# Kernel tuning notes

Measured on AMD Instinct MI355X. Metric: run time of the kernel, lower is better.

## Reference

```python
import jax, jax.numpy as jnp
import numpy as np

B, T, D, H = 4, 2048, 1024, 16
HD = D // H  # head_size = 64


def setup_inputs() -> dict:
    key = jax.random.key(0)
    ks = jax.random.split(key, 6)
    s = 0.02
    x = jax.random.normal(ks[0], (B, T, D), dtype=jnp.float32)
    # per-head unfused projections, stacked over heads: [H, D, HD]
    Wq = jax.random.normal(ks[1], (H, D, HD), dtype=jnp.float32) * s
    Wk = jax.random.normal(ks[2], (H, D, HD), dtype=jnp.float32) * s
    Wv = jax.random.normal(ks[3], (H, D, HD), dtype=jnp.float32) * s
    # output projection, torch Linear layout [out, in]
    Wo = jax.random.normal(ks[4], (D, D), dtype=jnp.float32) * s
    bo = jax.random.normal(ks[5], (D,), dtype=jnp.float32) * s
    return {"x": x, "Wq": Wq, "Wk": Wk, "Wv": Wv, "Wo": Wo, "bo": bo}


def reference(x, Wq, Wk, Wv, Wo, bo):
    b, t, d = x.shape
    hd = Wq.shape[-1]
    q = jnp.einsum('btd,hdk->bhtk', x, Wq)
    k = jnp.einsum('btd,hdk->bhtk', x, Wk)
    v = jnp.einsum('btd,hdk->bhtk', x, Wv)
    scores = jnp.einsum('bhtk,bhsk->bhts', q, k) / jnp.sqrt(jnp.float32(hd))
    mask = jnp.tril(jnp.ones((t, t), dtype=bool))  # causal
    scores = jnp.where(mask, scores, jnp.float32(-jnp.inf))
    p = jax.nn.softmax(scores, axis=-1)
    o = jnp.einsum('bhts,bhsk->bhtk', p, v)
    o = o.transpose(0, 2, 1, 3).reshape(b, t, d)  # concat heads
    return o @ Wo.T + bo
```

## Files before the change

kernel.cpp:

```cpp
#include <hip/hip_runtime.h>
#include <hip/hip_bf16.h>
#include <stdint.h>

#define B_   4
#define T_   2048
#define D_   1024
#define H_   16
#define HD_  64
#define MROWS (B_*T_)
#define NQKV  3072
#define NST  (T_/64)

typedef __attribute__((ext_vector_type(8))) short  short8;
typedef __attribute__((ext_vector_type(4))) short  bf16x4;
typedef __attribute__((ext_vector_type(4))) float  floatx4;

#define QSCALE 0.1803368801111244f

__device__ inline void async_copy16(const __hip_bfloat16* g, __hip_bfloat16* l) {
  __builtin_amdgcn_global_load_lds(
      (const __attribute__((address_space(1))) void*)g,
      (__attribute__((address_space(3))) void*)l, 16, 0, 0);
}

__device__ inline floatx4 mfma16(bf16x4 a, bf16x4 b, floatx4 c) {
#if __has_builtin(__builtin_amdgcn_mfma_f32_16x16x16bf16_1k)
  return __builtin_amdgcn_mfma_f32_16x16x16bf16_1k(a, b, c, 0, 0, 0);
#elif __has_builtin(__builtin_amdgcn_mfma_f32_16x16x16_bf16)
  return __builtin_amdgcn_mfma_f32_16x16x16_bf16(a, b, c, 0, 0, 0);
#else
  short8 a8 = (short8){a[0], a[1], a[2], a[3], 0, 0, 0, 0};
  short8 b8 = (short8){b[0], b[1], b[2], b[3], 0, 0, 0, 0};
  return __builtin_amdgcn_mfma_f32_16x16x32_bf16(a8, b8, c, 0, 0, 0);
#endif
}

__global__ void prep(const float* __restrict__ x, const float* __restrict__ Wo,
                     const float* __restrict__ Wq, const float* __restrict__ Wk,
                     const float* __restrict__ Wv,
                     __hip_bfloat16* __restrict__ xb, __hip_bfloat16* __restrict__ wob,
                     __hip_bfloat16* __restrict__ wqkv) {
  __shared__ __hip_bfloat16 tile[64][65];
  const int bid = (int)blockIdx.x;
  const int t = threadIdx.x;
  if (bid < 8192) {
    int i = (bid * 256 + t) * 4;
    float4 v = *(const float4*)(x + i);
    xb[i + 0] = __float2bfloat16(v.x);
    xb[i + 1] = __float2bfloat16(v.y);
    xb[i + 2] = __float2bfloat16(v.z);
    xb[i + 3] = __float2bfloat16(v.w);
  } else if (bid < 9216) {
    int i = ((bid - 8192) * 256 + t) * 4;
    float4 v = *(const float4*)(Wo + i);
    wob[i + 0] = __float2bfloat16(v.x);
    wob[i + 1] = __float2bfloat16(v.y);
    wob[i + 2] = __float2bfloat16(v.z);
    wob[i + 3] = __float2bfloat16(v.w);
  } else {
    int idx = bid - 9216;
    const int d0 = (idx & 15) * 64;
    const int wh = idx >> 4;
    const int which = wh >> 4, h = wh & 15;
    const float* W = (which == 0) ? Wq : ((which == 1) ? Wk : Wv);
    const float* base = W + (size_t)h * D_ * HD_;
#pragma unroll
    for (int i = 0; i < 16; i++) {
      int e = i * 256 + t;
      int dr = e >> 6, hd = e & 63;
      tile[dr][hd] = __float2bfloat16(base[(size_t)(d0 + dr) * HD_ + hd]);
    }
    __syncthreads();
#pragma unroll
    for (int i = 0; i < 16; i++) {
      int e = i * 256 + t;
      int hd = e >> 6, dr = e & 63;
      wqkv[(size_t)(which * 1024 + h * 64 + hd) * D_ + d0 + dr] = tile[dr][hd];
    }
  }
}

__global__ void repack_kv(const __hip_bfloat16* __restrict__ qkv,
                          __hip_bfloat16* __restrict__ kpack, __hip_bfloat16* __restrict__ vpack) {
  __shared__ __hip_bfloat16 Ks[64][72];
  __shared__ __hip_bfloat16 Vs[64][72];
  const int tid = threadIdx.x;
  const int st = blockIdx.x, bh = blockIdx.y;
  const int b = bh >> 4, h = bh & 15;
#pragma unroll
  for (int p = 0; p < 2; p++) {
    int c = p * 256 + tid;
    int row = c >> 3, col8 = c & 7;
    const __hip_bfloat16* src = qkv + (size_t)(b * T_ + st * 64 + row) * NQKV + h * HD_ + col8 * 8;
    *(uint4*)&Ks[row][col8 * 8] = *(const uint4*)(src + 1024);
    *(uint4*)&Vs[row][col8 * 8] = *(const uint4*)(src + 2048);
  }
  __syncthreads();
  const size_t base = ((size_t)bh * NST + st) * 8 * 512;
#pragma unroll
  for (int p = 0; p < 2; p++) {
    int pair = p * 256 + tid;
    int c = pair >> 6, l = pair & 63;
    int lq = l & 15, q = l >> 4;
    int ni = c >> 1, half = c & 1;
    short8 v = *(const short8*)&Ks[ni * 16 + lq][half * 32 + q * 8];
    *(short8*)(kpack + base + (size_t)c * 512 + l * 8) = v;
  }
#pragma unroll
  for (int p = 0; p < 2; p++) {
    int pair = p * 256 + tid;
    int c = pair >> 6, l = pair & 63;
    int lq = l & 15, q = l >> 4;
    int m = c >> 2, nt = c & 3;
    __hip_bfloat16 tmp[8];
#pragma unroll
    for (int half = 0; half < 2; half++)
#pragma unroll
      for (int j = 0; j < 4; j++)
        tmp[half * 4 + j] = Vs[(2 * m + half) * 16 + q * 4 + j][nt * 16 + lq];
    *(short8*)(vpack + base + (size_t)c * 512 + l * 8) = *(short8*)tmp;
  }
}


__device__ inline void stage16k(const __hip_bfloat16* __restrict__ grow0, int K,
                                short* ldst, int tid) {
#pragma unroll
  for (int l = 0; l < 2; ++l) {
    int c = l * 512 + tid;
    int r = c >> 3;
    int sw = (c & 7) ^ (r & 7);
    async_copy16(grow0 + (size_t)r * K + sw * 8, (__hip_bfloat16*)(ldst + c * 8));
  }
}

__device__ inline short8 fragld2(const short* base, int r, int slot) {
  return *(const short8*)(base + r * 64 + (((slot) ^ (r & 7)) << 3));
}

__launch_bounds__(512, 2)
__global__ void gemmq(const __hip_bfloat16* __restrict__ A, const __hip_bfloat16* __restrict__ Bt,
                      __hip_bfloat16* __restrict__ Cb, int M, int N, int K, float qscale) {
  __shared__ short LDS[2][32768];
  const int tid = threadIdx.x;
  const int lane = tid & 63, wid = tid >> 6;
  const int lq = lane & 15, quad = lane >> 4;
  const int wr = wid >> 2, wc = wid & 3;

  const int lin = (int)blockIdx.x;
  const int s = (lin & 7) * 64 + (lin >> 3);
  const int m0 = (s & 63) * 128, n0 = (s >> 6) * 384;

  const int NT = K >> 6;

  floatx4 acc[4][6];
#pragma unroll
  for (int i = 0; i < 4; i++)
#pragma unroll
    for (int j = 0; j < 6; j++) acc[i][j] = (floatx4){0.f, 0.f, 0.f, 0.f};

  {
    short* b0 = &LDS[0][0];
    stage16k(A + (size_t)m0 * K, K, b0, tid);
#pragma unroll
    for (int j = 0; j < 3; ++j)
      stage16k(Bt + (size_t)(n0 + 128 * j) * K, K, b0 + 8192 + 8192 * j, tid);
  }

#pragma unroll 1
  for (int t = 0; t < NT; ++t) {
    __syncthreads();
    const short* buf = &LDS[t & 1][0];
    short* nb = &LDS[(t & 1) ^ 1][0];
    const int kc = (t + 1) << 6;

    short8 a0[4], b0[6];
#pragma unroll
    for (int mi = 0; mi < 4; ++mi)
      a0[mi] = fragld2(buf, wr * 64 + mi * 16 + lq, quad);
#pragma unroll
    for (int ni = 0; ni < 6; ++ni)
      b0[ni] = fragld2(buf + 8192, wc * 96 + ni * 16 + lq, quad);
    if (t + 1 < NT) {
      stage16k(A + (size_t)m0 * K + kc, K, nb, tid);
#pragma unroll
      for (int j = 0; j < 3; ++j)
        stage16k(Bt + (size_t)(n0 + 128 * j) * K + kc, K, nb + 8192 + 8192 * j, tid);
    }
    __builtin_amdgcn_s_setprio(1);
#pragma unroll
    for (int mi = 0; mi < 4; ++mi)
#pragma unroll
      for (int ni = 0; ni < 6; ++ni)
        acc[mi][ni] = __builtin_amdgcn_mfma_f32_16x16x32_bf16(a0[mi], b0[ni], acc[mi][ni], 0, 0, 0);
    __builtin_amdgcn_s_setprio(0);

    short8 a1[4], b1[6];
#pragma unroll
    for (int mi = 0; mi < 4; ++mi)
      a1[mi] = fragld2(buf, wr * 64 + mi * 16 + lq, 4 + quad);
#pragma unroll
    for (int ni = 0; ni < 6; ++ni)
      b1[ni] = fragld2(buf + 8192, wc * 96 + ni * 16 + lq, 4 + quad);
    __builtin_amdgcn_s_setprio(1);
#pragma unroll
    for (int mi = 0; mi < 4; ++mi)
#pragma unroll
      for (int ni = 0; ni < 6; ++ni)
        acc[mi][ni] = __builtin_amdgcn_mfma_f32_16x16x32_bf16(a1[mi], b1[ni], acc[mi][ni], 0, 0, 0);
    __builtin_amdgcn_s_setprio(0);
  }

#pragma unroll
  for (int mi = 0; mi < 4; ++mi) {
#pragma unroll
    for (int ni = 0; ni < 6; ++ni) {
      int col = n0 + wc * 96 + ni * 16 + lq;
      float sc = (col < 1024) ? qscale : 1.0f;
#pragma unroll
      for (int r = 0; r < 4; ++r) {
        int row = m0 + wr * 64 + mi * 16 + quad * 4 + r;
        Cb[(size_t)row * N + col] = __float2bfloat16(acc[mi][ni][r] * sc);
      }
    }
  }
}

template <int EPI>
__launch_bounds__(256, 2)
__global__ void gemm_bt(const __hip_bfloat16* __restrict__ A, const __hip_bfloat16* __restrict__ Bt,
                        __hip_bfloat16* __restrict__ Cb, float* __restrict__ Cf,
                        const float* __restrict__ bias, int M, int N, int K, float qscale) {
  __shared__ __hip_bfloat16 As[128 * 32];
  __shared__ __hip_bfloat16 Bs[128 * 32];
  const int tid = threadIdx.x;
  const int w = tid >> 6, lane = tid & 63;
  const int lq = lane & 15, quad = lane >> 4;
  const int wr = w >> 1, wc = w & 1;
  const int m0 = blockIdx.x * 128, n0 = blockIdx.y * 128;

  floatx4 acc[4][4];
#pragma unroll
  for (int i = 0; i < 4; i++)
#pragma unroll
    for (int j = 0; j < 4; j++) acc[i][j] = (floatx4){0.f, 0.f, 0.f, 0.f};

  for (int k0 = 0; k0 < K; k0 += 32) {
    __syncthreads();
#pragma unroll
    for (int ph = 0; ph < 2; ++ph) {
      int c = ph * 256 + tid;
      int row = c >> 2, col8 = c & 3;
      async_copy16(A + (size_t)(m0 + row) * K + k0 + col8 * 8, As + c * 8);
      async_copy16(Bt + (size_t)(n0 + row) * K + k0 + col8 * 8, Bs + c * 8);
    }
    __syncthreads();
    short8 af[4], bf[4];
#pragma unroll
    for (int mi = 0; mi < 4; mi++)
      af[mi] = *(const short8*)(As + (wr * 64 + mi * 16 + lq) * 32 + quad * 8);
#pragma unroll
    for (int ni = 0; ni < 4; ni++)
      bf[ni] = *(const short8*)(Bs + (wc * 64 + ni * 16 + lq) * 32 + quad * 8);
#pragma unroll
    for (int mi = 0; mi < 4; mi++)
#pragma unroll
      for (int ni = 0; ni < 4; ni++)
        acc[mi][ni] = __builtin_amdgcn_mfma_f32_16x16x32_bf16(af[mi], bf[ni], acc[mi][ni], 0, 0, 0);
  }

#pragma unroll
  for (int mi = 0; mi < 4; mi++) {
#pragma unroll
    for (int ni = 0; ni < 4; ni++) {
      int col = n0 + wc * 64 + ni * 16 + lq;
      if (EPI == 0) {
        float s = (col < 1024) ? qscale : 1.0f;
#pragma unroll
        for (int r = 0; r < 4; r++) {
          int row = m0 + wr * 64 + mi * 16 + quad * 4 + r;
          Cb[(size_t)row * N + col] = __float2bfloat16(acc[mi][ni][r] * s);
        }
      } else {
        float bv = bias[col];
#pragma unroll
        for (int r = 0; r < 4; r++) {
          int row = m0 + wr * 64 + mi * 16 + quad * 4 + r;
          Cf[(size_t)row * N + col] = acc[mi][ni][r] + bv;
        }
      }
    }
  }
}

__launch_bounds__(256, 2)
__global__ void attn(const __hip_bfloat16* __restrict__ qkv,
                     const __hip_bfloat16* __restrict__ kpack,
                     const __hip_bfloat16* __restrict__ vpack,
                     __hip_bfloat16* __restrict__ obuf) {
  __shared__ __hip_bfloat16 KVs[2][8192];
  const int tid = threadIdx.x;
  const int w = tid >> 6, lane = tid & 63;
  const int lq = lane & 15, quad = lane >> 4;

  const int bh = (int)blockIdx.x;
  const int a  = (int)blockIdx.y;
  const int b = bh >> 4, h = bh & 15;

  const __hip_bfloat16* kbase = kpack + ((size_t)bh * NST) * 4096;
  const __hip_bfloat16* vbase = vpack + ((size_t)bh * NST) * 4096;

#pragma unroll 1
  for (int seg = 0; seg < 2; ++seg) {
    const int tbase = seg ? (NST - 2 - 2 * a) : (2 * a);
    const int qt = tbase + (w >> 1);
    const int rbase = (w & 1) * 32;

    short8 qf[2][2];
#pragma unroll
    for (int bi = 0; bi < 2; bi++) {
      const __hip_bfloat16* qp =
          qkv + ((size_t)(b * T_ + qt * 64 + rbase + bi * 16 + lq)) * NQKV + h * HD_;
      qf[bi][0] = *(const short8*)(qp + quad * 8);
      qf[bi][1] = *(const short8*)(qp + 32 + quad * 8);
    }

    floatx4 Oacc[2][4];
#pragma unroll
    for (int bi = 0; bi < 2; bi++)
#pragma unroll
      for (int i = 0; i < 4; i++) Oacc[bi][i] = (floatx4){0.f, 0.f, 0.f, 0.f};
    float lrow[2] = {0.f, 0.f};

    const int itTop = tbase + 1;

#pragma unroll
    for (int j = 0; j < 2; ++j) {
      int c = j * 256 + tid;
      async_copy16(kbase + (size_t)c * 8, &KVs[0][0] + c * 8);
      async_copy16(vbase + (size_t)c * 8, &KVs[0][4096] + c * 8);
    }
    __syncthreads();

#pragma unroll 1
    for (int it = 0; it <= itTop; ++it) {
      const int cur = it & 1;
      if (it < itTop) {
        const __hip_bfloat16* kn = kbase + (size_t)(it + 1) * 4096;
        const __hip_bfloat16* vn = vbase + (size_t)(it + 1) * 4096;
#pragma unroll
        for (int j = 0; j < 2; ++j) {
          int c = j * 256 + tid;
          async_copy16(kn + (size_t)c * 8, &KVs[cur ^ 1][0] + c * 8);
          async_copy16(vn + (size_t)c * 8, &KVs[cur ^ 1][4096] + c * 8);
        }
      }
      if (it <= qt) {
        const __hip_bfloat16* Kb = &KVs[cur][0] + lane * 8;
        const __hip_bfloat16* Vb = &KVs[cur][4096] + lane * 8;
        short8 kf[4], kg[4];
#pragma unroll
        for (int ni = 0; ni < 4; ni++) {
          kf[ni] = *(const short8*)(Kb + (size_t)(ni * 2 + 0) * 512);
          kg[ni] = *(const short8*)(Kb + (size_t)(ni * 2 + 1) * 512);
        }
        short8 vfr[8];
#pragma unroll
        for (int c = 0; c < 8; c++) vfr[c] = *(const short8*)(Vb + (size_t)c * 512);

        floatx4 Sc[2][4];
        __builtin_amdgcn_s_setprio(1);
#pragma unroll
        for (int bi = 0; bi < 2; bi++)
#pragma unroll
          for (int ni = 0; ni < 4; ni++) {
            floatx4 c0 = (floatx4){0.f, 0.f, 0.f, 0.f};
            c0 = __builtin_amdgcn_mfma_f32_16x16x32_bf16(kf[ni], qf[bi][0], c0, 0, 0, 0);
            c0 = __builtin_amdgcn_mfma_f32_16x16x32_bf16(kg[ni], qf[bi][1], c0, 0, 0, 0);
            Sc[bi][ni] = c0;
          }
        __builtin_amdgcn_s_setprio(0);

        if (it == qt) {
#pragma unroll
          for (int bi = 0; bi < 2; bi++) {
            int lrow_idx = rbase + bi * 16 + lq;
#pragma unroll
            for (int ni = 0; ni < 4; ni++)
#pragma unroll
              for (int r = 0; r < 4; r++) {
                int s_loc = ni * 16 + quad * 4 + r;
                if (s_loc > lrow_idx) Sc[bi][ni][r] = -__builtin_inff();
              }
          }
        }

        bf16x4 pf[2][4];
#pragma unroll
        for (int bi = 0; bi < 2; bi++)
#pragma unroll
          for (int c = 0; c < 4; c++) {
            __hip_bfloat16 pb[4];
#pragma unroll
            for (int r = 0; r < 4; r++) {
              float p = __builtin_amdgcn_exp2f(Sc[bi][c][r]);
              lrow[bi] += p;
              pb[r] = __float2bfloat16(p);
            }
            pf[bi][c] = *(bf16x4*)pb;
          }

        __builtin_amdgcn_s_setprio(1);
#pragma unroll
        for (int m = 0; m < 2; m++)
#pragma unroll
          for (int nt = 0; nt < 4; nt++) {
            short8 v8 = vfr[m * 4 + nt];
            bf16x4 vlo = (bf16x4){v8[0], v8[1], v8[2], v8[3]};
            bf16x4 vhi = (bf16x4){v8[4], v8[5], v8[6], v8[7]};
#pragma unroll
            for (int bi = 0; bi < 2; bi++) {
              Oacc[bi][nt] = mfma16(pf[bi][2 * m + 0], vlo, Oacc[bi][nt]);
              Oacc[bi][nt] = mfma16(pf[bi][2 * m + 1], vhi, Oacc[bi][nt]);
            }
          }
        __builtin_amdgcn_s_setprio(0);
      }
      __syncthreads();
    }

#pragma unroll
    for (int bi = 0; bi < 2; bi++) {
      float ps = lrow[bi];
      ps += __shfl_xor(ps, 16);
      ps += __shfl_xor(ps, 32);
      float inv = 1.0f / ps;
#pragma unroll
      for (int r = 0; r < 4; r++) {
        float invr = __shfl(inv, quad * 4 + r);
        int t = qt * 64 + rbase + bi * 16 + quad * 4 + r;
#pragma unroll
        for (int nt = 0; nt < 4; nt++)
          obuf[(size_t)(b * T_ + t) * D_ + h * HD_ + nt * 16 + lq] =
              __float2bfloat16(Oacc[bi][nt][r] * invr);
      }
    }
  }
}


extern "C" void kernel_launch(void* const* d_in, const int* in_sizes, int n_in,
                              void* d_out, int out_size, void* d_ws, size_t ws_size,
                              hipStream_t stream) {
  const float* x  = (const float*)d_in[0];
  const float* Wq = (const float*)d_in[1];
  const float* Wk = (const float*)d_in[2];
  const float* Wv = (const float*)d_in[3];
  const float* Wo = (const float*)d_in[4];
  const float* bo = (const float*)d_in[5];
  float* out = (float*)d_out;

  char* ws = (char*)d_ws;
  __hip_bfloat16* xb    = (__hip_bfloat16*)(ws);
  __hip_bfloat16* obuf  = (__hip_bfloat16*)(ws);
  __hip_bfloat16* wqkv  = (__hip_bfloat16*)(ws + ((size_t)16 << 20));
  __hip_bfloat16* wob   = (__hip_bfloat16*)(ws + ((size_t)22 << 20));
  __hip_bfloat16* qkv   = (__hip_bfloat16*)(ws + ((size_t)24 << 20));
  __hip_bfloat16* kpack = (__hip_bfloat16*)(ws + ((size_t)72 << 20));
  __hip_bfloat16* vpack = (__hip_bfloat16*)(ws + ((size_t)88 << 20));

  prep<<<9984, 256, 0, stream>>>(x, Wo, Wq, Wk, Wv, xb, wob, wqkv);

  gemmq<<<512, 512, 0, stream>>>(xb, wqkv, qkv, MROWS, NQKV, D_, QSCALE);

  repack_kv<<<dim3(NST, B_ * H_), 256, 0, stream>>>(qkv, kpack, vpack);

  attn<<<dim3(B_ * H_, 8), 256, 0, stream>>>(qkv, kpack, vpack, obuf);

  gemm_bt<1><<<dim3(MROWS / 128, D_ / 128), 256, 0, stream>>>(
      obuf, wob, nullptr, out, bo, MROWS, D_, D_, 1.0f);
}
```

Measured before the change: 237.4 us.

## Rewrite output projection GEMM with double-buffered 128x256 tiles and swizzled grid

Replaces the simple single-buffered 128x128 output-projection GEMM with a 512-thread kernel that computes 128x256 tiles. It uses K=64 steps and double-buffered LDS staging, so the next tile's global-to-LDS loads overlap the current MFMAs. The grid is remapped with an XCD-style swizzle for cache locality, and MFMA sections get raised wave priority. This cuts sync overhead and load stalls, but uses more LDS per block (96KB), which may limit occupancy.

Measured after the change: 247.9 us. +4.4%, slower.

```diff
diff --git a/kernel.cpp b/kernel.cpp
--- a/kernel.cpp
+++ b/kernel.cpp
@@ -226,18 +226,21 @@
   }
 }
 
-template <int EPI>
-__launch_bounds__(256, 2)
-__global__ void gemm_bt(const __hip_bfloat16* __restrict__ A, const __hip_bfloat16* __restrict__ Bt,
-                        __hip_bfloat16* __restrict__ Cb, float* __restrict__ Cf,
-                        const float* __restrict__ bias, int M, int N, int K, float qscale) {
-  __shared__ __hip_bfloat16 As[128 * 32];
-  __shared__ __hip_bfloat16 Bs[128 * 32];
+__launch_bounds__(512, 2)
+__global__ void gemmo(const __hip_bfloat16* __restrict__ A, const __hip_bfloat16* __restrict__ Bt,
+                      float* __restrict__ Cf, const float* __restrict__ bias,
+                      int M, int N, int K) {
+  __shared__ short LDS[2][24576];
   const int tid = threadIdx.x;
-  const int w = tid >> 6, lane = tid & 63;
+  const int lane = tid & 63, wid = tid >> 6;
   const int lq = lane & 15, quad = lane >> 4;
-  const int wr = w >> 1, wc = w & 1;
-  const int m0 = blockIdx.x * 128, n0 = blockIdx.y * 128;
+  const int wr = wid >> 2, wc = wid & 3;
+
+  const int lin = (int)blockIdx.x;
+  const int s = (lin & 7) * 32 + (lin >> 3);
+  const int m0 = (s & 63) * 128, n0 = (s >> 6) * 256;
+
+  const int NT = K >> 6;
 
   floatx4 acc[4][4];
 #pragma unroll
@@ -245,49 +248,66 @@
 #pragma unroll
     for (int j = 0; j < 4; j++) acc[i][j] = (floatx4){0.f, 0.f, 0.f, 0.f};
 
-  for (int k0 = 0; k0 < K; k0 += 32) {
+  {
+    short* b0 = &LDS[0][0];
+    stage16k(A + (size_t)m0 * K, K, b0, tid);
+    stage16k(Bt + (size_t)n0 * K, K, b0 + 8192, tid);
+    stage16k(Bt + (size_t)(n0 + 128) * K, K, b0 + 16384, tid);
+  }
+
+#pragma unroll 1
+  for (int t = 0; t < NT; ++t) {
     __syncthreads();
-#pragma unroll
-    for (int ph = 0; ph < 2; ++ph) {
-      int c = ph * 256 + tid;
-      int row = c >> 2, col8 = c & 3;
-      async_copy16(A + (size_t)(m0 + row) * K + k0 + col8 * 8, As + c * 8);
-      async_copy16(Bt + (size_t)(n0 + row) * K + k0 + col8 * 8, Bs + c * 8);
-    }
-    __syncthreads();
-    short8 af[4], bf[4];
-#pragma unroll
-    for (int mi = 0; mi < 4; mi++)
-      af[mi] = *(const short8*)(As + (wr * 64 + mi * 16 + lq) * 32 + quad * 8);
-#pragma unroll
-    for (int ni = 0; ni < 4; ni++)
-      bf[ni] = *(const short8*)(Bs + (wc * 64 + ni * 16 + lq) * 32 + quad * 8);
-#pragma unroll
-    for (int mi = 0; mi < 4; mi++)
-#pragma unroll
-      for (int ni = 0; ni < 4; ni++)
-        acc[mi][ni] = __builtin_amdgcn_mfma_f32_16x16x32_bf16(af[mi], bf[ni], acc[mi][ni], 0, 0, 0);
-  }
-
-#pragma unroll
-  for (int mi = 0; mi < 4; mi++) {
-#pragma unroll
-    for (int ni = 0; ni < 4; ni++) {
+    const short* buf = &LDS[t & 1][0];
+    short* nb = &LDS[(t & 1) ^ 1][0];
+    const int kc = (t + 1) << 6;
+
+    short8 a0[4], b0[4];
+#pragma unroll
+    for (int mi = 0; mi < 4; ++mi)
+      a0[mi] = fragld2(buf, wr * 64 + mi * 16 + lq, quad);
+#pragma unroll
+    for (int ni = 0; ni < 4; ++ni)
+      b0[ni] = fragld2(buf + 8192, wc * 64 + ni * 16 + lq, quad);
+    if (t + 1 < NT) {
+      stage16k(A + (size_t)m0 * K + kc, K, nb, tid);
+      stage16k(Bt + (size_t)n0 * K + kc, K, nb + 8192, tid);
+      stage16k(Bt + (size_t)(n0 + 128) * K + kc, K, nb + 16384, tid);
+    }
+    __builtin_amdgcn_s_setprio(1);
+#pragma unroll
+    for (int mi = 0; mi < 4; ++mi)
+#pragma unroll
+      for (int ni = 0; ni < 4; ++ni)
+        acc[mi][ni] = __builtin_amdgcn_mfma_f32_16x16x32_bf16(a0[mi], b0[ni], acc[mi][ni], 0, 0, 0);
+    __builtin_amdgcn_s_setprio(0);
+
+    short8 a1[4], b1[4];
+#pragma unroll
+    for (int mi = 0; mi < 4; ++mi)
+      a1[mi] = fragld2(buf, wr * 64 + mi * 16 + lq, 4 + quad);
+#pragma unroll
+    for (int ni = 0; ni < 4; ++ni)
+      b1[ni] = fragld2(buf + 8192, wc * 64 + ni * 16 + lq, 4 + quad);
+    __builtin_amdgcn_s_setprio(1);
+#pragma unroll
+    for (int mi = 0; mi < 4; ++mi)
+#pragma unroll
+      for (int ni = 0; ni < 4; ++ni)
+        acc[mi][ni] = __builtin_amdgcn_mfma_f32_16x16x32_bf16(a1[mi], b1[ni], acc[mi][ni], 0, 0, 0);
+    __builtin_amdgcn_s_setprio(0);
+  }
+
+#pragma unroll
+  for (int mi = 0; mi < 4; ++mi) {
+#pragma unroll
+    for (int ni = 0; ni < 4; ++ni) {
       int col = n0 + wc * 64 + ni * 16 + lq;
-      if (EPI == 0) {
-        float s = (col < 1024) ? qscale : 1.0f;
-#pragma unroll
-        for (int r = 0; r < 4; r++) {
-          int row = m0 + wr * 64 + mi * 16 + quad * 4 + r;
-          Cb[(size_t)row * N + col] = __float2bfloat16(acc[mi][ni][r] * s);
-        }
-      } else {
-        float bv = bias[col];
-#pragma unroll
-        for (int r = 0; r < 4; r++) {
-          int row = m0 + wr * 64 + mi * 16 + quad * 4 + r;
-          Cf[(size_t)row * N + col] = acc[mi][ni][r] + bv;
-        }
+      float bv = bias[col];
+#pragma unroll
+      for (int r = 0; r < 4; ++r) {
+        int row = m0 + wr * 64 + mi * 16 + quad * 4 + r;
+        Cf[(size_t)row * N + col] = acc[mi][ni][r] + bv;
       }
     }
   }
@@ -477,6 +497,5 @@
 
   attn<<<dim3(B_ * H_, 8), 256, 0, stream>>>(qkv, kpack, vpack, obuf);
 
-  gemm_bt<1><<<dim3(MROWS / 128, D_ / 128), 256, 0, stream>>>(
-      obuf, wob, nullptr, out, bo, MROWS, D_, D_, 1.0f);
-}
+  gemmo<<<256, 512, 0, stream>>>(obuf, wob, out, bo, MROWS, D_, D_);
+}
```

## Stage two 64-key tiles per pipeline step in attention loop

Applied to the files above, without the earlier changes.

The attention kernel now loads two 64-row K/V tiles per double-buffered stage (doubling LDS to 64 KB), so it does half as many barrier-separated iterations. It processes both tiles from the current buffer before synchronising. The generic __syncthreads is replaced by an explicit vmcnt(0) wait plus a raw s_barrier. This is meant to cut synchronisation and prefetch-issue overhead, but the larger LDS use may reduce the number of blocks resident per CU.

Result: no change. 233.7 us (-1.6%).

```diff
diff --git a/kernel.cpp b/kernel.cpp
--- a/kernel.cpp
+++ b/kernel.cpp
@@ -298,7 +298,7 @@
                      const __hip_bfloat16* __restrict__ kpack,
                      const __hip_bfloat16* __restrict__ vpack,
                      __hip_bfloat16* __restrict__ obuf) {
-  __shared__ __hip_bfloat16 KVs[2][8192];
+  __shared__ __hip_bfloat16 KVs[2][16384];
   const int tid = threadIdx.x;
   const int w = tid >> 6, lane = tid & 63;
   const int lq = lane & 15, quad = lane >> 4;
@@ -332,101 +332,108 @@
       for (int i = 0; i < 4; i++) Oacc[bi][i] = (floatx4){0.f, 0.f, 0.f, 0.f};
     float lrow[2] = {0.f, 0.f};
 
-    const int itTop = tbase + 1;
-
-#pragma unroll
-    for (int j = 0; j < 2; ++j) {
+    const int pTop = tbase >> 1;
+
+#pragma unroll
+    for (int j = 0; j < 4; ++j) {
       int c = j * 256 + tid;
       async_copy16(kbase + (size_t)c * 8, &KVs[0][0] + c * 8);
-      async_copy16(vbase + (size_t)c * 8, &KVs[0][4096] + c * 8);
-    }
-    __syncthreads();
-
+      async_copy16(vbase + (size_t)c * 8, &KVs[0][8192] + c * 8);
+    }
+    asm volatile("s_waitcnt vmcnt(0)" ::: "memory");
+    __builtin_amdgcn_s_barrier();
+
+    int cur = 0;
 #pragma unroll 1
-    for (int it = 0; it <= itTop; ++it) {
-      const int cur = it & 1;
-      if (it < itTop) {
-        const __hip_bfloat16* kn = kbase + (size_t)(it + 1) * 4096;
-        const __hip_bfloat16* vn = vbase + (size_t)(it + 1) * 4096;
-#pragma unroll
-        for (int j = 0; j < 2; ++j) {
+    for (int p = 0; p <= pTop; ++p) {
+      if (p < pTop) {
+        const __hip_bfloat16* kn = kbase + (size_t)(2 * (p + 1)) * 4096;
+        const __hip_bfloat16* vn = vbase + (size_t)(2 * (p + 1)) * 4096;
+#pragma unroll
+        for (int j = 0; j < 4; ++j) {
           int c = j * 256 + tid;
           async_copy16(kn + (size_t)c * 8, &KVs[cur ^ 1][0] + c * 8);
-          async_copy16(vn + (size_t)c * 8, &KVs[cur ^ 1][4096] + c * 8);
+          async_copy16(vn + (size_t)c * 8, &KVs[cur ^ 1][8192] + c * 8);
         }
       }
-      if (it <= qt) {
-        const __hip_bfloat16* Kb = &KVs[cur][0] + lane * 8;
-        const __hip_bfloat16* Vb = &KVs[cur][4096] + lane * 8;
-        short8 kf[4], kg[4];
-#pragma unroll
-        for (int ni = 0; ni < 4; ni++) {
-          kf[ni] = *(const short8*)(Kb + (size_t)(ni * 2 + 0) * 512);
-          kg[ni] = *(const short8*)(Kb + (size_t)(ni * 2 + 1) * 512);
-        }
-        short8 vfr[8];
-#pragma unroll
-        for (int c = 0; c < 8; c++) vfr[c] = *(const short8*)(Vb + (size_t)c * 512);
-
-        floatx4 Sc[2][4];
-        __builtin_amdgcn_s_setprio(1);
-#pragma unroll
-        for (int bi = 0; bi < 2; bi++)
+#pragma unroll
+      for (int f = 0; f < 2; ++f) {
+        const int t64 = 2 * p + f;
+        if (t64 <= qt) {
+          const __hip_bfloat16* Kb = &KVs[cur][f * 4096] + lane * 8;
+          const __hip_bfloat16* Vb = &KVs[cur][8192 + f * 4096] + lane * 8;
+          short8 kf[4], kg[4];
 #pragma unroll
           for (int ni = 0; ni < 4; ni++) {
-            floatx4 c0 = (floatx4){0.f, 0.f, 0.f, 0.f};
-            c0 = __builtin_amdgcn_mfma_f32_16x16x32_bf16(kf[ni], qf[bi][0], c0, 0, 0, 0);
-            c0 = __builtin_amdgcn_mfma_f32_16x16x32_bf16(kg[ni], qf[bi][1], c0, 0, 0, 0);
-            Sc[bi][ni] = c0;
+            kf[ni] = *(const short8*)(Kb + (size_t)(ni * 2 + 0) * 512);
+            kg[ni] = *(const short8*)(Kb + (size_t)(ni * 2 + 1) * 512);
           }
-        __builtin_amdgcn_s_setprio(0);
-
-        if (it == qt) {
-#pragma unroll
-          for (int bi = 0; bi < 2; bi++) {
-            int lrow_idx = rbase + bi * 16 + lq;
-#pragma unroll
-            for (int ni = 0; ni < 4; ni++)
-#pragma unroll
-              for (int r = 0; r < 4; r++) {
-                int s_loc = ni * 16 + quad * 4 + r;
-                if (s_loc > lrow_idx) Sc[bi][ni][r] = -__builtin_inff();
-              }
-          }
-        }
-
-        bf16x4 pf[2][4];
-#pragma unroll
-        for (int bi = 0; bi < 2; bi++)
-#pragma unroll
-          for (int c = 0; c < 4; c++) {
-            __hip_bfloat16 pb[4];
-#pragma unroll
-            for (int r = 0; r < 4; r++) {
-              float p = __builtin_amdgcn_exp2f(Sc[bi][c][r]);
-              lrow[bi] += p;
-              pb[r] = __float2bfloat16(p);
+          short8 vfr[8];
+#pragma unroll
+          for (int c = 0; c < 8; c++) vfr[c] = *(const short8*)(Vb + (size_t)c * 512);
+
+          floatx4 Sc[2][4];
+          __builtin_amdgcn_s_setprio(1);
+#pragma unroll
+          for (int bi = 0; bi < 2; bi++)
+#pragma unroll
+            for (int ni = 0; ni < 4; ni++) {
+              floatx4 c0 = (floatx4){0.f, 0.f, 0.f, 0.f};
+              c0 = __builtin_amdgcn_mfma_f32_16x16x32_bf16(kf[ni], qf[bi][0], c0, 0, 0, 0);
+              c0 = __builtin_amdgcn_mfma_f32_16x16x32_bf16(kg[ni], qf[bi][1], c0, 0, 0, 0);
+              Sc[bi][ni] = c0;
             }
-            pf[bi][c] = *(bf16x4*)pb;
-          }
-
-        __builtin_amdgcn_s_setprio(1);
-#pragma unroll
-        for (int m = 0; m < 2; m++)
-#pragma unroll
-          for (int nt = 0; nt < 4; nt++) {
-            short8 v8 = vfr[m * 4 + nt];
-            bf16x4 vlo = (bf16x4){v8[0], v8[1], v8[2], v8[3]};
-            bf16x4 vhi = (bf16x4){v8[4], v8[5], v8[6], v8[7]};
+          __builtin_amdgcn_s_setprio(0);
+
+          if (t64 == qt) {
 #pragma unroll
             for (int bi = 0; bi < 2; bi++) {
-              Oacc[bi][nt] = mfma16(pf[bi][2 * m + 0], vlo, Oacc[bi][nt]);
-              Oacc[bi][nt] = mfma16(pf[bi][2 * m + 1], vhi, Oacc[bi][nt]);
+              int lrow_idx = rbase + bi * 16 + lq;
+#pragma unroll
+              for (int ni = 0; ni < 4; ni++)
+#pragma unroll
+                for (int r = 0; r < 4; r++) {
+                  int s_loc = ni * 16 + quad * 4 + r;
+                  if (s_loc > lrow_idx) Sc[bi][ni][r] = -__builtin_inff();
+                }
             }
           }
-        __builtin_amdgcn_s_setprio(0);
+
+          bf16x4 pf[2][4];
+#pragma unroll
+          for (int bi = 0; bi < 2; bi++)
+#pragma unroll
+            for (int c = 0; c < 4; c++) {
+              __hip_bfloat16 pb[4];
+#pragma unroll
+              for (int r = 0; r < 4; r++) {
+                float pv = __builtin_amdgcn_exp2f(Sc[bi][c][r]);
+                lrow[bi] += pv;
+                pb[r] = __float2bfloat16(pv);
+              }
+              pf[bi][c] = *(bf16x4*)pb;
+            }
+
+          __builtin_amdgcn_s_setprio(1);
+#pragma unroll
+          for (int m = 0; m < 2; m++)
+#pragma unroll
+            for (int nt = 0; nt < 4; nt++) {
+              short8 v8 = vfr[m * 4 + nt];
+              bf16x4 vlo = (bf16x4){v8[0], v8[1], v8[2], v8[3]};
+              bf16x4 vhi = (bf16x4){v8[4], v8[5], v8[6], v8[7]};
+#pragma unroll
+              for (int bi = 0; bi < 2; bi++) {
+                Oacc[bi][nt] = mfma16(pf[bi][2 * m + 0], vlo, Oacc[bi][nt]);
+                Oacc[bi][nt] = mfma16(pf[bi][2 * m + 1], vhi, Oacc[bi][nt]);
+              }
+            }
+          __builtin_amdgcn_s_setprio(0);
+        }
       }
-      __syncthreads();
+      if (p < pTop) { asm volatile("s_waitcnt vmcnt(0)" ::: "memory"); }
+      __builtin_amdgcn_s_barrier();
+      cur ^= 1;
     }
 
 #pragma unroll
```
